# Kernel optimization log

Measured on AMD Instinct MI355X. Metric: run time of the kernel, lower is better.

## Reference

```python
import jax, jax.numpy as jnp
import numpy as np

B, L, C, H = 2, 2048, 2048, 16
COND = 2048
HID = 4 * C
LN_EPS = 1e-6


def _ln(x):
    m = jnp.mean(x, axis=-1, keepdims=True)
    v = jnp.mean((x - m) ** 2, axis=-1, keepdims=True)
    return (x - m) / jnp.sqrt(v + LN_EPS)


def _gelu_tanh(u):
    c = np.sqrt(2.0 / np.pi).astype(np.float32)
    return 0.5 * u * (1.0 + jnp.tanh(c * (u + 0.044715 * u ** 3)))


def setup_inputs() -> dict:
    key = jax.random.key(0)
    ks = jax.random.split(key, 8)
    s = 0.02
    return {
        "x": jax.random.normal(ks[0], (B, L, C), jnp.float32),
        "cond_BD": jax.random.normal(ks[1], (B, COND), jnp.float32),
        "attn_bias": jnp.zeros((1, 1, L, L), jnp.float32),
        "Wqkv": (jax.random.normal(ks[2], (3 * C, C), jnp.float32) * s),
        "q_bias": jnp.zeros((C,), jnp.float32),
        "v_bias": jnp.zeros((C,), jnp.float32),
        "scale_mul_log": jnp.full((1, H, 1, 1), np.log(4.0), jnp.float32),
        "Wproj": (jax.random.normal(ks[3], (C, C), jnp.float32) * s),
        "bproj": jnp.zeros((C,), jnp.float32),
        "Wada": (jax.random.normal(ks[4], (6 * C, COND), jnp.float32) * s),
        "bada": jnp.zeros((6 * C,), jnp.float32),
        "Wfc1": (jax.random.normal(ks[5], (HID, C), jnp.float32) * s),
        "bfc1": jnp.zeros((HID,), jnp.float32),
        "Wfc2": (jax.random.normal(ks[6], (C, HID), jnp.float32) * s),
        "bfc2": jnp.zeros((C,), jnp.float32),
    }


def reference(x, cond_BD, attn_bias, Wqkv, q_bias, v_bias, scale_mul_log,
              Wproj, bproj, Wada, bada, Wfc1, bfc1, Wfc2, bfc2):
    Bs, Lx, Cx = x.shape
    D = Cx // H
    # AdaLN modulation: SiLU -> Linear(cond_dim, 6C) -> view(B,1,6,C).unbind(2)
    ada = (jax.nn.silu(cond_BD) @ Wada.T + bada).reshape(Bs, 1, 6, Cx)
    gamma1, gamma2, scale1, scale2, shift1, shift2 = [ada[:, :, i, :] for i in range(6)]

    def attn(xin):
        qkv_bias = jnp.concatenate([q_bias, jnp.zeros_like(q_bias), v_bias])
        qkv = (xin @ Wqkv.T + qkv_bias).reshape(Bs, Lx, 3, H, D)
        qkv = jnp.transpose(qkv, (2, 0, 3, 1, 4))  # [3, B, H, L, D]
        q, k, v = qkv[0], qkv[1], qkv[2]
        # cos-attn: L2-normalize q,k; q scaled by exp(clamped log-scale); softmax scale = 1
        sm = jnp.exp(jnp.minimum(scale_mul_log, jnp.log(jnp.float32(100.0))))
        qn = q / jnp.maximum(jnp.linalg.norm(q, axis=-1, keepdims=True), 1e-12) * sm
        kn = k / jnp.maximum(jnp.linalg.norm(k, axis=-1, keepdims=True), 1e-12)
        scores = jnp.einsum('bhqd,bhkd->bhqk', qn, kn) + attn_bias
        p = jax.nn.softmax(scores, axis=-1)
        o = jnp.einsum('bhqk,bhkd->bhqd', p, v)
        o = jnp.transpose(o, (0, 2, 1, 3)).reshape(Bs, Lx, Cx)
        return o @ Wproj.T + bproj

    x = x + attn(_ln(x) * (scale1 + 1.0) + shift1) * gamma1
    h = _gelu_tanh((_ln(x) * (scale2 + 1.0) + shift2) @ Wfc1.T + bfc1)
    x = x + (h @ Wfc2.T + bfc2) * gamma2
    return x
```

## Files before the change

### kernel.cpp

```cpp
#include <hip/hip_runtime.h>

typedef unsigned short u16;
typedef float f32x4 __attribute__((ext_vector_type(4)));
typedef short short8 __attribute__((ext_vector_type(8)));

#define C_ 2048
#define L_ 2048
#define H_ 16
#define D_ 128
#define SIXC 12288

__device__ __forceinline__ u16 f2bf(float f) {
  union { float f; unsigned u; } v; v.f = f;
  unsigned r = v.u + 0x7FFFu + ((v.u >> 16) & 1u);
  return (u16)(r >> 16);
}
__device__ __forceinline__ float bf2f(u16 b) {
  union { unsigned u; float f; } v; v.u = ((unsigned)b) << 16; return v.f;
}

#define GLOAD_LDS16(g, l)                                            \
  __builtin_amdgcn_global_load_lds(                                  \
      (__attribute__((address_space(1))) void*)(g),                  \
      (__attribute__((address_space(3))) void*)(l), 16, 0, 0)

template <int N> __device__ __forceinline__ void wait_vmcnt() {
  if constexpr (N == 8)      asm volatile("s_waitcnt vmcnt(8)" ::: "memory");
  else if constexpr (N == 6) asm volatile("s_waitcnt vmcnt(6)" ::: "memory");
  else                       asm volatile("s_waitcnt vmcnt(0)" ::: "memory");
}

#define NQKV 12582912
#define NPRJ 4194304
#define NFC1 16777216
#define NFC2 16777216
__global__ __launch_bounds__(256) void conv_all(
    const float* __restrict__ wqkv, const float* __restrict__ wproj,
    const float* __restrict__ wfc1, const float* __restrict__ wfc2,
    u16* __restrict__ oqkv, u16* __restrict__ oproj,
    u16* __restrict__ ofc1, u16* __restrict__ ofc2) {
  int i = (blockIdx.x * 256 + threadIdx.x) * 4;
  const float* src; u16* dst; int off;
  if (i < NQKV) { src = wqkv; dst = oqkv; off = i; }
  else if (i < NQKV + NPRJ) { src = wproj; dst = oproj; off = i - NQKV; }
  else if (i < NQKV + NPRJ + NFC1) { src = wfc1; dst = ofc1; off = i - NQKV - NPRJ; }
  else { src = wfc2; dst = ofc2; off = i - NQKV - NPRJ - NFC1; }
  float4 v = *(const float4*)&src[off];
  ushort4 o;
  o.x = f2bf(v.x); o.y = f2bf(v.y); o.z = f2bf(v.z); o.w = f2bf(v.w);
  *(ushort4*)&dst[off] = o;
}

__global__ __launch_bounds__(256) void prep_kernel(
    const float* __restrict__ cond, const float* __restrict__ qb,
    const float* __restrict__ vb, const float* __restrict__ sml,
    float* __restrict__ silu_cond, float* __restrict__ qkvbias,
    float* __restrict__ sm, int* __restrict__ bflag) {
  int i = blockIdx.x * 256 + threadIdx.x;
  if (i == 0) bflag[0] = 0;
  if (i < 4096) { float c = cond[i]; silu_cond[i] = c / (1.f + __expf(-c)); }
  if (i < 6144) {
    float bv = (i < 2048) ? qb[i] : ((i < 4096) ? 0.f : vb[i - 4096]);
    qkvbias[i] = bv;
  }
  if (i < 16) sm[i] = __expf(fminf(sml[i], 4.6051701859880914f));
}

__global__ __launch_bounds__(256) void bias_check(
    const float* __restrict__ b, int* __restrict__ flag) {
  int i = (blockIdx.x * 256 + threadIdx.x) * 4;
  float4 v = *(const float4*)&b[i];
  bool nz = (v.x != 0.f) | (v.y != 0.f) | (v.z != 0.f) | (v.w != 0.f);
  if (__any(nz) && (threadIdx.x & 63) == 0) atomicOr(flag, 1);
}

__global__ __launch_bounds__(256) void ada_gemm(
    const float* __restrict__ sc, const float* __restrict__ Wada,
    const float* __restrict__ bada, float* __restrict__ ada) {
  int gw = (blockIdx.x * 256 + threadIdx.x) >> 6;
  int lane = threadIdx.x & 63;
  int b = gw / SIXC, row = gw % SIXC;
  const float* s0 = sc + b * 2048;
  const float* w0 = Wada + (size_t)row * 2048;
  float s = 0.f;
  for (int k = lane * 4; k < 2048; k += 256) {
    float4 a = *(const float4*)&s0[k];
    float4 w = *(const float4*)&w0[k];
    s = fmaf(a.x, w.x, s); s = fmaf(a.y, w.y, s);
    s = fmaf(a.z, w.z, s); s = fmaf(a.w, w.w, s);
  }
  #pragma unroll
  for (int off = 32; off; off >>= 1) s += __shfl_xor(s, off);
  if (lane == 0) ada[(size_t)b * SIXC + row] = s + bada[row];
}

__global__ __launch_bounds__(256) void ln_mod(
    const float* __restrict__ x, const float* __restrict__ ada,
    u16* __restrict__ out, int soff, int shoff) {
  int r = blockIdx.x;
  int b = r >> 11;
  int tid = threadIdx.x;
  const float* xr = x + (size_t)r * 2048;
  int c0 = tid * 8;
  float4 u0 = *(const float4*)&xr[c0];
  float4 u1 = *(const float4*)&xr[c0 + 4];
  float v[8] = {u0.x,u0.y,u0.z,u0.w,u1.x,u1.y,u1.z,u1.w};
  float s = 0.f, s2 = 0.f;
  #pragma unroll
  for (int j = 0; j < 8; ++j) { s += v[j]; s2 = fmaf(v[j], v[j], s2); }
  int wv = tid >> 6, lane = tid & 63;
  #pragma unroll
  for (int off = 32; off; off >>= 1) { s += __shfl_xor(s, off); s2 += __shfl_xor(s2, off); }
  __shared__ float red[8];
  if (!lane) { red[wv] = s; red[4 + wv] = s2; }
  __syncthreads();
  s = red[0] + red[1] + red[2] + red[3];
  s2 = red[4] + red[5] + red[6] + red[7];
  float mean = s * (1.f / 2048.f);
  float var = s2 * (1.f / 2048.f) - mean * mean;
  float rstd = rsqrtf(var + 1e-6f);
  const float* sc = ada + (size_t)b * SIXC + soff;
  const float* sh = ada + (size_t)b * SIXC + shoff;
  u16* orow = out + (size_t)r * 2048;
  #pragma unroll
  for (int j = 0; j < 8; ++j) {
    int c = c0 + j;
    float y = (v[j] - mean) * rstd * (1.f + sc[c]) + sh[c];
    orow[c] = f2bf(y);
  }
}

__global__ __launch_bounds__(256) void qk_norm_bf(
    u16* __restrict__ qb, u16* __restrict__ kb, const float* __restrict__ sm) {
  int gw = (blockIdx.x * 256 + threadIdx.x) >> 6;
  int lane = threadIdx.x & 63;
  int which = gw >> 16;
  int rid = gw & 0xFFFF;
  int h = (rid >> 11) & 15;
  u16* base = (which ? kb : qb) + (size_t)rid * 128 + lane * 2;
  unsigned uu = *(const unsigned*)base;
  float v0 = bf2f((u16)(uu & 0xFFFFu));
  float v1 = bf2f((u16)(uu >> 16));
  float ss = v0 * v0 + v1 * v1;
  #pragma unroll
  for (int off = 32; off; off >>= 1) ss += __shfl_xor(ss, off);
  float rn = 1.f / fmaxf(sqrtf(ss), 1e-12f);
  if (which == 0) rn *= sm[h];
  unsigned o = (unsigned)f2bf(v0 * rn) | ((unsigned)f2bf(v1 * rn) << 16);
  *(unsigned*)base = o;
}

#define PSP 68
__global__ __launch_bounds__(256) void attn_mfma(
    const u16* __restrict__ qb, const u16* __restrict__ kb,
    const u16* __restrict__ vbt, const float* __restrict__ bias,
    const int* __restrict__ bflag, u16* __restrict__ o) {
  __shared__ u16 Ks[2][64 * 128];
  __shared__ u16 Vt[2][128 * 64];
  __shared__ u16 Ps[4][16 * PSP];
  int tid = threadIdx.x;
  int w = tid >> 6, lane = tid & 63;
  int flat = blockIdx.y * gridDim.x + blockIdx.x;
  int rl = (flat & 7) * 128 + (flat >> 3);
  int bh = rl >> 5, b = bh >> 4, h = bh & 15;
  int q0 = (rl & 31) * 64;
  int lr = lane & 15, lg = lane >> 4;
  const int hasb = bflag[0];
  short8 aq[4];
  {
    const u16* qrow = qb + ((size_t)bh * L_ + q0 + w * 16 + lr) * 128 + lg * 8;
    #pragma unroll
    for (int ks = 0; ks < 4; ++ks) aq[ks] = *(const short8*)(qrow + ks * 32);
  }
  f32x4 oacc[8] = {};
  float m = -1e30f, l = 0.f;
  const float* brow = bias + (size_t)(q0 + w * 16 + lr) * L_;
  const u16* kbase = kb + (size_t)bh * L_ * 128;
  const u16* vbase = vbt + (size_t)bh * 128 * L_;
  const int kq0 = tid;
  const int vq0 = tid;

  float4 brg[4], bnr[4];
  #pragma unroll
  for (int i = 0; i < 4; ++i) {
    int q = i * 256 + kq0;
    int r = q >> 4, c = q & 15;
    GLOAD_LDS16(kbase + (size_t)r * 128 + ((c ^ (r & 7)) * 8), &Ks[0][q * 8]);
  }
  #pragma unroll
  for (int i = 0; i < 4; ++i) {
    int q = i * 256 + vq0;
    int r = q >> 3, c = q & 7;
    GLOAD_LDS16(vbase + (size_t)r * L_ + ((c ^ (r & 7)) * 8), &Vt[0][q * 8]);
  }
  #pragma unroll
  for (int kg = 0; kg < 4; ++kg) {
    if (hasb) brg[kg] = *(const float4*)&brow[kg * 16 + lg * 4];
    else { brg[kg].x = 0.f; brg[kg].y = 0.f; brg[kg].z = 0.f; brg[kg].w = 0.f; }
    bnr[kg].x = 0.f; bnr[kg].y = 0.f; bnr[kg].z = 0.f; bnr[kg].w = 0.f;
  }
  __syncthreads();

  for (int kt = 0; kt < 32; ++kt) {
    const int cur = kt & 1;
    if (kt < 31) {
      const int nxt = cur ^ 1;
      const u16* kb2 = kbase + (size_t)(kt + 1) * 64 * 128;
      #pragma unroll
      for (int i = 0; i < 4; ++i) {
        int q = i * 256 + kq0;
        int r = q >> 4, c = q & 15;
        GLOAD_LDS16(kb2 + (size_t)r * 128 + ((c ^ (r & 7)) * 8), &Ks[nxt][q * 8]);
      }
      #pragma unroll
      for (int i = 0; i < 4; ++i) {
        int q = i * 256 + vq0;
        int r = q >> 3, c = q & 7;
        GLOAD_LDS16(vbase + (size_t)r * L_ + (kt + 1) * 64 + ((c ^ (r & 7)) * 8),
                    &Vt[nxt][q * 8]);
      }
      if (hasb) {
        #pragma unroll
        for (int kg = 0; kg < 4; ++kg)
          bnr[kg] = *(const float4*)&brow[(kt + 1) * 64 + kg * 16 + lg * 4];
      }
    }
    f32x4 s[4] = {};
    __builtin_amdgcn_s_setprio(1);
    #pragma unroll
    for (int ks = 0; ks < 4; ++ks) {
      #pragma unroll
      for (int kg = 0; kg < 4; ++kg) {
        int row = kg * 16 + lr;
        short8 bk = *(const short8*)&Ks[cur][row * 128 + (((ks * 4 + lg) ^ (lr & 7)) * 8)];
        s[kg] = __builtin_amdgcn_mfma_f32_16x16x32_bf16(bk, aq[ks], s[kg], 0, 0, 0);
      }
    }
    __builtin_amdgcn_s_setprio(0);
    float p[4][4];
    #pragma unroll
    for (int kg = 0; kg < 4; ++kg) {
      p[kg][0] = s[kg][0] + brg[kg].x;
      p[kg][1] = s[kg][1] + brg[kg].y;
      p[kg][2] = s[kg][2] + brg[kg].z;
      p[kg][3] = s[kg][3] + brg[kg].w;
    }
    float tm = fmaxf(
        fmaxf(fmaxf(fmaxf(p[0][0], p[0][1]), fmaxf(p[0][2], p[0][3])),
              fmaxf(fmaxf(p[1][0], p[1][1]), fmaxf(p[1][2], p[1][3]))),
        fmaxf(fmaxf(fmaxf(p[2][0], p[2][1]), fmaxf(p[2][2], p[2][3])),
              fmaxf(fmaxf(p[3][0], p[3][1]), fmaxf(p[3][2], p[3][3]))));
    tm = fmaxf(tm, __shfl_xor(tm, 16));
    tm = fmaxf(tm, __shfl_xor(tm, 32));
    if (__any(tm > m + 8.f)) {
      float nm = fmaxf(m, tm);
      float a = __expf(m - nm);
      m = nm;
      l *= a;
      float al[4];
      #pragma unroll
      for (int j = 0; j < 4; ++j) al[j] = __shfl(a, lg * 4 + j);
      #pragma unroll
      for (int dg = 0; dg < 8; ++dg) {
        f32x4 t = oacc[dg];
        t[0] *= al[0]; t[1] *= al[1]; t[2] *= al[2]; t[3] *= al[3];
        oacc[dg] = t;
      }
    }
    float ps = 0.f;
    #pragma unroll
    for (int kg = 0; kg < 4; ++kg) {
      #pragma unroll
      for (int j = 0; j < 4; ++j) { p[kg][j] = __expf(p[kg][j] - m); ps += p[kg][j]; }
    }
    ps += __shfl_xor(ps, 16);
    ps += __shfl_xor(ps, 32);
    l += ps;
    #pragma unroll
    for (int kg = 0; kg < 4; ++kg) {
      unsigned lo = (unsigned)f2bf(p[kg][0]) | ((unsigned)f2bf(p[kg][1]) << 16);
      unsigned hi = (unsigned)f2bf(p[kg][2]) | ((unsigned)f2bf(p[kg][3]) << 16);
      uint2 w2; w2.x = lo; w2.y = hi;
      *(uint2*)&Ps[w][lr * PSP + kg * 16 + lg * 4] = w2;
    }
    __threadfence_block();
    short8 pa0 = *(const short8*)&Ps[w][lr * PSP + lg * 8];
    short8 pa1 = *(const short8*)&Ps[w][lr * PSP + 32 + lg * 8];
    __builtin_amdgcn_s_setprio(1);
    #pragma unroll
    for (int dg = 0; dg < 8; ++dg) {
      int row = dg * 16 + lr;
      short8 bv0 = *(const short8*)&Vt[cur][row * 64 + ((lg ^ (lr & 7)) * 8)];
      oacc[dg] = __builtin_amdgcn_mfma_f32_16x16x32_bf16(pa0, bv0, oacc[dg], 0, 0, 0);
      short8 bv1 = *(const short8*)&Vt[cur][row * 64 + (((4 + lg) ^ (lr & 7)) * 8)];
      oacc[dg] = __builtin_amdgcn_mfma_f32_16x16x32_bf16(pa1, bv1, oacc[dg], 0, 0, 0);
    }
    __builtin_amdgcn_s_setprio(0);
    __syncthreads();
    #pragma unroll
    for (int i = 0; i < 4; ++i) brg[i] = bnr[i];
  }
  float inv[4];
  #pragma unroll
  for (int j = 0; j < 4; ++j) inv[j] = 1.f / __shfl(l, lg * 4 + j);
  #pragma unroll
  for (int j = 0; j < 4; ++j) {
    u16* dst = &o[((size_t)(b * L_) + q0 + w * 16 + lg * 4 + j) * 2048 + h * 128 + lr];
    #pragma unroll
    for (int dg = 0; dg < 8; ++dg) dst[dg * 16] = f2bf(oacc[dg][j] * inv[j]);
  }
}

#define RD_A(cur, mh)                                                         \
  _Pragma("unroll") for (int kk = 0; kk < 2; ++kk) {                          \
    const int col_ = (kk * 32 + lg * 8) ^ cswz;                               \
    _Pragma("unroll") for (int i = 0; i < 4; ++i)                             \
      af[i][kk] = *(const short8*)                                            \
          &As[cur][(wr * 128 + (mh) * 64 + i * 16 + lr) * 64 + col_];         \
  }
#define RD_B(cur, nh, BB)                                                     \
  _Pragma("unroll") for (int kk = 0; kk < 2; ++kk) {                          \
    const int col_ = (kk * 32 + lg * 8) ^ cswz;                               \
    _Pragma("unroll") for (int j = 0; j < 2; ++j)                             \
      BB[j][kk] = *(const short8*)                                            \
          &Bs[cur][(wc * 64 + (nh) * 32 + j * 16 + lr) * 64 + col_];          \
  }
#define MMQ(mh, nh, BB)                                                       \
  __builtin_amdgcn_s_setprio(1);                                              \
  _Pragma("unroll") for (int kk = 0; kk < 2; ++kk)                            \
  _Pragma("unroll") for (int i = 0; i < 4; ++i)                               \
  _Pragma("unroll") for (int j = 0; j < 2; ++j)                               \
    acc[(mh) * 4 + i][(nh) * 2 + j] = __builtin_amdgcn_mfma_f32_16x16x32_bf16(\
        af[i][kk], BB[j][kk], acc[(mh) * 4 + i][(nh) * 2 + j], 0, 0, 0);      \
  __builtin_amdgcn_s_setprio(0);
#define LGKM0 asm volatile("s_waitcnt lgkmcnt(0)" ::: "memory")

template <int EPI>
__global__ __launch_bounds__(512, 2) void gemm256(
    const u16* __restrict__ A, const u16* __restrict__ W,
    const float* __restrict__ bias,
    u16* __restrict__ outb,
    u16* __restrict__ p0, u16* __restrict__ p1, u16* __restrict__ p2,
    int M, int N, int K, int lda) {
  __shared__ __attribute__((aligned(16))) u16 As[2][256 * 64];
  __shared__ __attribute__((aligned(16))) u16 Bs[2][256 * 64];
  const int tid = threadIdx.x;
  int my = blockIdx.y, half = 0;
  if constexpr (EPI == 3) { half = my >> 4; my &= 15; }
  const int m0 = my * 256, n0 = blockIdx.x * 256;
  const int wv = tid >> 6, lane = tid & 63;
  const int wr = wv >> 2, wc = wv & 3;
  const int lr = lane & 15, lg = lane >> 4;
  const int sr = lane >> 3;
  const int scol = ((lane & 7) ^ sr) * 8;
  const int cswz = (lr & 7) * 8;
  f32x4 acc[8][4] = {};
  const u16* Ab = A + (size_t)m0 * lda + (size_t)half * K;
  const u16* Bb = W + (size_t)n0 * lda + (size_t)half * K;
  const int nt = K >> 6;

  auto stA2 = [&](int bi, int k0, int sel) {
    #pragma unroll
    for (int q = 0; q < 2; ++q) {
      int c = wv * 2 + q;
      int chunk = sel == 0 ? (c < 8 ? c : c + 8)
                           : (c < 8 ? c + 8 : c + 16);
      int row = chunk * 8 + sr;
      GLOAD_LDS16(Ab + (size_t)row * lda + k0 + scol, &As[bi][chunk * 512]);
    }
  };
  auto stA4 = [&](int bi, int k0) {
    #pragma unroll
    for (int q = 0; q < 4; ++q) {
      int chunk = wv * 4 + q, row = chunk * 8 + sr;
      GLOAD_LDS16(Ab + (size_t)row * lda + k0 + scol, &As[bi][chunk * 512]);
    }
  };
  auto stB4 = [&](int bi, int k0) {
    #pragma unroll
    for (int q = 0; q < 4; ++q) {
      int chunk = wv * 4 + q, row = chunk * 8 + sr;
      GLOAD_LDS16(Bb + (size_t)row * lda + k0 + scol, &Bs[bi][chunk * 512]);
    }
  };

  short8 af[4][2], bfl[2][2], bfh[2][2];
  stA4(0, 0); stB4(0, 0);
  stA4(1, 64); stB4(1, 64);
  wait_vmcnt<8>();
  __builtin_amdgcn_s_barrier();

  for (int t = 0; t < nt; ++t) {
    const int cur = t & 1;
    const int k2 = (t + 2) << 6;
    const bool st = t + 2 < nt;
    RD_A(cur, 0); RD_B(cur, 0, bfl);
    __builtin_amdgcn_s_barrier();
    LGKM0;
    MMQ(0, 0, bfl);
    __builtin_amdgcn_s_barrier();
    RD_B(cur, 1, bfh);
    __builtin_amdgcn_s_barrier();
    LGKM0;
    if (st) stA2(cur, k2, 0);
    MMQ(0, 1, bfh);
    __builtin_amdgcn_s_barrier();
    RD_A(cur, 1);
    __builtin_amdgcn_s_barrier();
    LGKM0;
    if (st) stB4(cur, k2);
    MMQ(1, 0, bfl);
    __builtin_amdgcn_s_barrier();
    __builtin_amdgcn_sched_barrier(0x10F);
    if (st) { stA2(cur, k2, 1); wait_vmcnt<8>(); }
    else if (t + 1 < nt) { wait_vmcnt<0>(); }
    MMQ(1, 1, bfh);
    __builtin_amdgcn_s_barrier();
  }

  #pragma unroll
  for (int mi = 0; mi < 8; ++mi) {
    #pragma unroll
    for (int ni = 0; ni < 4; ++ni) {
      int gcol = n0 + wc * 64 + ni * 16 + lr;
      float bv = (EPI == 3) ? 0.f : bias[gcol];
      #pragma unroll
      for (int j = 0; j < 4; ++j) {
        int grow = m0 + wr * 128 + mi * 16 + lg * 4 + j;
        float v = acc[mi][ni][j] + bv;
        if constexpr (EPI == 0) {
          int which = gcol >> 11;
          int h = (gcol >> 7) & 15;
          int d = gcol & 127;
          int b = grow >> 11, ll = grow & 2047;
          int bh = b * 16 + h;
          if (which == 0)      p0[((size_t)bh * L_ + ll) * 128 + d] = f2bf(v);
          else if (which == 1) p1[((size_t)bh * L_ + ll) * 128 + d] = f2bf(v);
          else                 p2[((size_t)bh * 128 + d) * L_ + ll] = f2bf(v);
        } else if constexpr (EPI == 1) {
          float u = 0.7978845608028654f * (v + 0.044715f * v * v * v);
          float e = __expf(2.f * u);
          float th = 1.f - 2.f / (e + 1.f);
          outb[(size_t)grow * N + gcol] = f2bf(0.5f * v * (1.f + th));
        } else {
          u16* pd = half ? p1 : p0;
          pd[(size_t)grow * N + gcol] = f2bf(v);
        }
      }
    }
  }
}

__global__ __launch_bounds__(256) void fc2_combine(
    const u16* __restrict__ pa, const u16* __restrict__ pb,
    const float* __restrict__ bias, const float* __restrict__ res,
    const float* __restrict__ ada, float* __restrict__ out) {
  int i = (blockIdx.x * 256 + threadIdx.x) * 4;
  int col = i & 2047;
  int b = i >> 22;
  ushort4 a4 = *(const ushort4*)&pa[i];
  ushort4 b4 = *(const ushort4*)&pb[i];
  float4 r = *(const float4*)&res[i];
  const float* ad = ada + (size_t)b * SIXC + C_;
  float4 o;
  o.x = r.x + (bf2f(a4.x) + bf2f(b4.x) + bias[col])     * ad[col];
  o.y = r.y + (bf2f(a4.y) + bf2f(b4.y) + bias[col + 1]) * ad[col + 1];
  o.z = r.z + (bf2f(a4.z) + bf2f(b4.z) + bias[col + 2]) * ad[col + 2];
  o.w = r.w + (bf2f(a4.w) + bf2f(b4.w) + bias[col + 3]) * ad[col + 3];
  *(float4*)&out[i] = o;
}

template <int EPI>
__global__ __launch_bounds__(256) void gemm128(
    const u16* __restrict__ A, const u16* __restrict__ W,
    const float* __restrict__ bias, const float* __restrict__ res,
    const float* __restrict__ ada, int goff,
    float* __restrict__ outf, u16* __restrict__ outb,
    int M, int N, int K) {
  __shared__ u16 As[2][128 * 64];
  __shared__ u16 Bs[2][128 * 64];
  const int tid = threadIdx.x;
  const int m0 = blockIdx.y * 128, n0 = blockIdx.x * 128;
  const int wv = tid >> 6, lane = tid & 63;
  const int wr = wv >> 1, wc = wv & 1;
  const int lr = lane & 15, lg = lane >> 4;
  const int sr = lane >> 3;
  const int scol = ((lane & 7) ^ sr) * 8;
  const int cswz = (lr & 7) * 8;
  f32x4 acc[4][4] = {};
  const u16* Ab = A + (size_t)m0 * K;
  const u16* Bb = W + (size_t)n0 * K;
  const int nt = K >> 6;
  auto stage = [&](int bi, int k0) {
    #pragma unroll
    for (int p = 0; p < 4; ++p) {
      int chunk = wv * 4 + p;
      int row = chunk * 8 + sr;
      GLOAD_LDS16(Ab + (size_t)row * K + k0 + scol, &As[bi][chunk * 512]);
      GLOAD_LDS16(Bb + (size_t)row * K + k0 + scol, &Bs[bi][chunk * 512]);
    }
  };
  stage(0, 0);
  stage(1, 64);
  for (int t = 0; t < nt; ++t) {
    const int cur = t & 1;
    if (t + 1 < nt) wait_vmcnt<8>(); else wait_vmcnt<0>();
    __builtin_amdgcn_s_barrier();
    __builtin_amdgcn_sched_barrier(0);
    #pragma unroll
    for (int kk = 0; kk < 2; ++kk) {
      short8 af[4], bfr[4];
      const int col = (kk * 32 + lg * 8) ^ cswz;
      #pragma unroll
      for (int i = 0; i < 4; ++i) {
        af[i]  = *(const short8*)&As[cur][(wr * 64 + i * 16 + lr) * 64 + col];
        bfr[i] = *(const short8*)&Bs[cur][(wc * 64 + i * 16 + lr) * 64 + col];
      }
      #pragma unroll
      for (int mi = 0; mi < 4; ++mi)
        #pragma unroll
        for (int ni = 0; ni < 4; ++ni)
          acc[mi][ni] = __builtin_amdgcn_mfma_f32_16x16x32_bf16(af[mi], bfr[ni], acc[mi][ni], 0, 0, 0);
    }
    __builtin_amdgcn_sched_barrier(0);
    asm volatile("s_waitcnt lgkmcnt(0)" ::: "memory");
    __builtin_amdgcn_s_barrier();
    __builtin_amdgcn_sched_barrier(0);
    if (t + 2 < nt) stage(cur, (t + 2) << 6);
  }
  #pragma unroll
  for (int mi = 0; mi < 4; ++mi) {
    #pragma unroll
    for (int ni = 0; ni < 4; ++ni) {
      int gcol = n0 + wc * 64 + ni * 16 + lr;
      float bv = bias[gcol];
      #pragma unroll
      for (int j = 0; j < 4; ++j) {
        int grow = m0 + wr * 64 + mi * 16 + lg * 4 + j;
        float v = acc[mi][ni][j] + bv;
        if (EPI == 1) {
          float u = 0.7978845608028654f * (v + 0.044715f * v * v * v);
          float e = __expf(2.f * u);
          float th = 1.f - 2.f / (e + 1.f);
          outb[(size_t)grow * N + gcol] = f2bf(0.5f * v * (1.f + th));
        } else {
          int b = grow >> 11;
          float g = ada[(size_t)b * SIXC + goff + gcol];
          size_t oi = (size_t)grow * N + gcol;
          outf[oi] = res[oi] + v * g;
        }
      }
    }
  }
}

extern "C" void kernel_launch(void* const* d_in, const int* in_sizes, int n_in,
                              void* d_out, int out_size, void* d_ws, size_t ws_size,
                              hipStream_t stream) {
  const float* x        = (const float*)d_in[0];
  const float* cond     = (const float*)d_in[1];
  const float* attnbias = (const float*)d_in[2];
  const float* Wqkv     = (const float*)d_in[3];
  const float* q_bias   = (const float*)d_in[4];
  const float* v_bias   = (const float*)d_in[5];
  const float* sml      = (const float*)d_in[6];
  const float* Wproj    = (const float*)d_in[7];
  const float* bproj    = (const float*)d_in[8];
  const float* Wada     = (const float*)d_in[9];
  const float* bada     = (const float*)d_in[10];
  const float* Wfc1     = (const float*)d_in[11];
  const float* bfc1     = (const float*)d_in[12];
  const float* Wfc2     = (const float*)d_in[13];
  const float* bfc2     = (const float*)d_in[14];
  float* out = (float*)d_out;
  char* ws = (char*)d_ws;
  const size_t MB = 1ull << 20;

  float* silu_cond = (float*)(ws + 0);
  float* qkvbias   = (float*)(ws + (16 << 10));
  float* smbuf     = (float*)(ws + (40 << 10));
  int*   bflag     = (int*)(ws + (44 << 10));
  float* adab      = (float*)(ws + (48 << 10));
  u16*   xob       = (u16*)(ws + 1 * MB);
  u16*   qbb       = (u16*)(ws + 17 * MB);
  u16*   kbb       = (u16*)(ws + 33 * MB);
  float* x1        = (float*)(ws + 17 * MB);
  u16*   vbt       = (u16*)(ws + 49 * MB);
  u16*   hbuf      = (u16*)(ws + 49 * MB);
  u16*   wqkv_bf   = (u16*)(ws + 65 * MB);
  u16*   wproj_bf  = (u16*)(ws + 89 * MB);
  u16*   wfc1_bf   = (u16*)(ws + 113 * MB);
  u16*   wfc2_bf   = (u16*)(ws + 145 * MB);
  u16*   pa        = (u16*)(ws + 1 * MB);
  u16*   pb        = (u16*)(ws + 113 * MB);

  conv_all<<<49152, 256, 0, stream>>>(Wqkv, Wproj, Wfc1, Wfc2,
                                      wqkv_bf, wproj_bf, wfc1_bf, wfc2_bf);
  prep_kernel<<<24, 256, 0, stream>>>(cond, q_bias, v_bias, sml, silu_cond,
                                      qkvbias, smbuf, bflag);
  bias_check<<<4096, 256, 0, stream>>>(attnbias, bflag);
  ada_gemm<<<6144, 256, 0, stream>>>(silu_cond, Wada, bada, adab);
  ln_mod<<<4096, 256, 0, stream>>>(x, adab, xob, 2 * C_, 4 * C_);
  gemm256<0><<<dim3(24, 16), 512, 0, stream>>>(xob, wqkv_bf, qkvbias,
      nullptr, qbb, kbb, vbt, 4096, 6144, 2048, 2048);
  qk_norm_bf<<<32768, 256, 0, stream>>>(qbb, kbb, smbuf);
  attn_mfma<<<dim3(32, 32), 256, 0, stream>>>(qbb, kbb, vbt, attnbias, bflag, xob);
  gemm128<2><<<dim3(16, 32), 256, 0, stream>>>(xob, wproj_bf, bproj, x, adab, 0,
      x1, nullptr, 4096, 2048, 2048);
  ln_mod<<<4096, 256, 0, stream>>>(x1, adab, xob, 3 * C_, 5 * C_);
  gemm256<1><<<dim3(32, 16), 512, 0, stream>>>(xob, wfc1_bf, bfc1,
      hbuf, nullptr, nullptr, nullptr, 4096, 8192, 2048, 2048);
  gemm256<3><<<dim3(8, 32), 512, 0, stream>>>(hbuf, wfc2_bf, bfc2,
      nullptr, pa, pb, nullptr, 4096, 2048, 4096, 8192);
  fc2_combine<<<8192, 256, 0, stream>>>(pa, pb, bfc2, x1, adab, out);
}
```

Before: 769.4 us.

## Restructure GEMM main loop to read full k-slices then issue all MFMAs with fewer barriers

Reworks the 256x256 GEMM inner loop. All of the A and B LDS fragments for a k-tile are now read into registers up front, gated by partial lgkmcnt waits and sched_barriers, and the 64 MFMAs run in four blocks of 16. Global-to-LDS staging of the tile two steps ahead is moved to a single point after the end-of-iteration barrier. This replaces the old interleaving, which used many barriers and split staging into halves. The aim is fewer workgroup barriers and better overlap of LDS reads with MFMA, at the cost of more fragment registers and less overlap of global loads with compute inside each iteration.

```diff
diff --git a/kernel.cpp b/kernel.cpp
--- a/kernel.cpp
+++ b/kernel.cpp
@@ -311,29 +311,24 @@
   }
 }
 
-#define RD_A(cur, mh)                                                         \
-  _Pragma("unroll") for (int kk = 0; kk < 2; ++kk) {                          \
-    const int col_ = (kk * 32 + lg * 8) ^ cswz;                               \
-    _Pragma("unroll") for (int i = 0; i < 4; ++i)                             \
-      af[i][kk] = *(const short8*)                                            \
-          &As[cur][(wr * 128 + (mh) * 64 + i * 16 + lr) * 64 + col_];         \
-  }
-#define RD_B(cur, nh, BB)                                                     \
-  _Pragma("unroll") for (int kk = 0; kk < 2; ++kk) {                          \
-    const int col_ = (kk * 32 + lg * 8) ^ cswz;                               \
-    _Pragma("unroll") for (int j = 0; j < 2; ++j)                             \
-      BB[j][kk] = *(const short8*)                                            \
-          &Bs[cur][(wc * 64 + (nh) * 32 + j * 16 + lr) * 64 + col_];          \
-  }
-#define MMQ(mh, nh, BB)                                                       \
+#define SB0 __builtin_amdgcn_sched_barrier(0)
+#define LGKM(N) asm volatile("s_waitcnt lgkmcnt(" #N ")" ::: "memory")
+
+#define RD_A4(cur, mh, kk, DST)                                               \
+  _Pragma("unroll") for (int i = 0; i < 4; ++i)                               \
+    DST[i] = *(const short8*)&As[cur][(wr * 128 + (mh) * 64 + i * 16 + lr) * 64 \
+                                      + (((kk) * 32 + lg * 8) ^ cswz)];
+#define RD_B4(cur, kk, DST)                                                   \
+  _Pragma("unroll") for (int j = 0; j < 4; ++j)                               \
+    DST[j] = *(const short8*)&Bs[cur][(wc * 64 + j * 16 + lr) * 64            \
+                                      + (((kk) * 32 + lg * 8) ^ cswz)];
+#define MM16(mh, AF, BF)                                                      \
   __builtin_amdgcn_s_setprio(1);                                              \
-  _Pragma("unroll") for (int kk = 0; kk < 2; ++kk)                            \
   _Pragma("unroll") for (int i = 0; i < 4; ++i)                               \
-  _Pragma("unroll") for (int j = 0; j < 2; ++j)                               \
-    acc[(mh) * 4 + i][(nh) * 2 + j] = __builtin_amdgcn_mfma_f32_16x16x32_bf16(\
-        af[i][kk], BB[j][kk], acc[(mh) * 4 + i][(nh) * 2 + j], 0, 0, 0);      \
+  _Pragma("unroll") for (int j = 0; j < 4; ++j)                               \
+    acc[(mh) * 4 + i][j] = __builtin_amdgcn_mfma_f32_16x16x32_bf16(           \
+        AF[i], BF[j], acc[(mh) * 4 + i][j], 0, 0, 0);                         \
   __builtin_amdgcn_s_setprio(0);
-#define LGKM0 asm volatile("s_waitcnt lgkmcnt(0)" ::: "memory")
 
 template <int EPI>
 __global__ __launch_bounds__(512, 2) void gemm256(
@@ -359,24 +354,12 @@
   const u16* Bb = W + (size_t)n0 * lda + (size_t)half * K;
   const int nt = K >> 6;
 
-  auto stA2 = [&](int bi, int k0, int sel) {
-    #pragma unroll
-    for (int q = 0; q < 2; ++q) {
-      int c = wv * 2 + q;
-      int chunk = sel == 0 ? (c < 8 ? c : c + 8)
-                           : (c < 8 ? c + 8 : c + 16);
-      int row = chunk * 8 + sr;
-      GLOAD_LDS16(Ab + (size_t)row * lda + k0 + scol, &As[bi][chunk * 512]);
-    }
-  };
-  auto stA4 = [&](int bi, int k0) {
+  auto stage = [&](int bi, int k0) {
     #pragma unroll
     for (int q = 0; q < 4; ++q) {
       int chunk = wv * 4 + q, row = chunk * 8 + sr;
       GLOAD_LDS16(Ab + (size_t)row * lda + k0 + scol, &As[bi][chunk * 512]);
     }
-  };
-  auto stB4 = [&](int bi, int k0) {
     #pragma unroll
     for (int q = 0; q < 4; ++q) {
       int chunk = wv * 4 + q, row = chunk * 8 + sr;
@@ -384,38 +367,33 @@
     }
   };
 
-  short8 af[4][2], bfl[2][2], bfh[2][2];
-  stA4(0, 0); stB4(0, 0);
-  stA4(1, 64); stB4(1, 64);
-  wait_vmcnt<8>();
-  __builtin_amdgcn_s_barrier();
+  short8 a0[4], a1[4], a2[4], a3[4], b0[4], b1[4];
+  stage(0, 0);
+  stage(1, 64);
 
   for (int t = 0; t < nt; ++t) {
     const int cur = t & 1;
-    const int k2 = (t + 2) << 6;
-    const bool st = t + 2 < nt;
-    RD_A(cur, 0); RD_B(cur, 0, bfl);
+    if (t + 1 < nt) wait_vmcnt<8>(); else wait_vmcnt<0>();
     __builtin_amdgcn_s_barrier();
-    LGKM0;
-    MMQ(0, 0, bfl);
+    SB0;
+    RD_A4(cur, 0, 0, a0); RD_B4(cur, 0, b0);
+    SB0;
+    RD_A4(cur, 0, 1, a1); RD_B4(cur, 1, b1);
+    SB0;
+    LGKM(8); SB0;
+    MM16(0, a0, b0);
+    SB0;
+    RD_A4(cur, 1, 0, a2); RD_A4(cur, 1, 1, a3);
+    SB0;
+    LGKM(8); SB0;
+    MM16(0, a1, b1);
+    LGKM(0); SB0;
+    MM16(1, a2, b0);
+    MM16(1, a3, b1);
+    SB0;
     __builtin_amdgcn_s_barrier();
-    RD_B(cur, 1, bfh);
-    __builtin_amdgcn_s_barrier();
-    LGKM0;
-    if (st) stA2(cur, k2, 0);
-    MMQ(0, 1, bfh);
-    __builtin_amdgcn_s_barrier();
-    RD_A(cur, 1);
-    __builtin_amdgcn_s_barrier();
-    LGKM0;
-    if (st) stB4(cur, k2);
-    MMQ(1, 0, bfl);
-    __builtin_amdgcn_s_barrier();
-    __builtin_amdgcn_sched_barrier(0x10F);
-    if (st) { stA2(cur, k2, 1); wait_vmcnt<8>(); }
-    else if (t + 1 < nt) { wait_vmcnt<0>(); }
-    MMQ(1, 1, bfh);
-    __builtin_amdgcn_s_barrier();
+    SB0;
+    if (t + 2 < nt) stage(cur, (t + 2) << 6);
   }
 
   #pragma unroll
```

After: 784.2 us. About the same (+1.9%).
